# Kernel tuning notes

Hardware: AMD Instinct MI355X
Metric: run time of the kernel (lower is better)

Reference implementation:

```python
import jax, jax.numpy as jnp
import numpy as np

N_USER, N_ITEM, D, K, E = 80000, 40000, 128, 10, 2000000

def _mlp(x, w1, b1, w2, b2, w3, b3):
    # MLP from source: linear->tanh->linear->tanh->linear->L2 normalize (eval mode, dropout off)
    x = jnp.tanh(x @ w1 + b1)
    x = jnp.tanh(x @ w2 + b2)
    x = x @ w3 + b3
    return x / jnp.maximum(jnp.linalg.norm(x, axis=-1, keepdims=True), 1e-12)

def setup_inputs() -> dict:
    key = jax.random.key(0)
    ks = jax.random.split(key, 24)
    s = 0.05
    inp = {
        'uemb_s': jax.random.normal(ks[0], (N_USER, D), jnp.float32),
        'iemb_s': jax.random.normal(ks[1], (N_ITEM, D), jnp.float32),
        'uemb_t': jax.random.normal(ks[2], (N_USER, D), jnp.float32),
        'u_emb_sp': jax.random.normal(ks[3], (N_USER, D), jnp.float32),
        'edge_user': jax.random.randint(ks[4], (E,), 0, N_USER, jnp.int32),
        'edge_item': jax.random.randint(ks[5], (E,), 0, N_ITEM, jnp.int32),
        # meta nets
        'Wu': jax.random.normal(ks[6], (4 * D, D), jnp.float32) * s,
        'bu': jnp.zeros((D,), jnp.float32),
        'Wi': jax.random.normal(ks[7], (2 * D, D), jnp.float32) * s,
        'bi': jnp.zeros((D,), jnp.float32),
        # mlp1: D -> D*K -> D//2 -> D*K
        'm1w1': jax.random.normal(ks[8], (D, D * K), jnp.float32) * s,
        'm1b1': jnp.zeros((D * K,), jnp.float32),
        'm1w2': jax.random.normal(ks[9], (D * K, D // 2), jnp.float32) * s,
        'm1b2': jnp.zeros((D // 2,), jnp.float32),
        'm1w3': jax.random.normal(ks[10], (D // 2, D * K), jnp.float32) * s,
        'm1b3': jnp.zeros((D * K,), jnp.float32),
        # mlp2: D -> D*K -> D//2 -> D*K
        'm2w1': jax.random.normal(ks[11], (D, D * K), jnp.float32) * s,
        'm2b1': jnp.zeros((D * K,), jnp.float32),
        'm2w2': jax.random.normal(ks[12], (D * K, D // 2), jnp.float32) * s,
        'm2b2': jnp.zeros((D // 2,), jnp.float32),
        'm2w3': jax.random.normal(ks[13], (D // 2, D * K), jnp.float32) * s,
        'm2b3': jnp.zeros((D * K,), jnp.float32),
    }
    return inp

def reference(uemb_s, iemb_s, uemb_t, u_emb_sp, edge_user, edge_item,
              Wu, bu, Wi, bi,
              m1w1, m1b1, m1w2, m1b2, m1w3, m1b3,
              m2w1, m2b1, m2w2, m2b2, m2w3, m2b3):
    # spmm with all-ones values == gather + segment_sum over the bipartite edge list
    neighbors_u = jax.ops.segment_sum(iemb_s[edge_item], edge_user, num_segments=N_USER)  # [U, D]
    tmp_embu = jax.lax.stop_gradient(
        jnp.concatenate([uemb_s, uemb_t, u_emb_sp, neighbors_u], axis=1)) @ Wu + bu       # [U, D]
    neighbors_i = jax.ops.segment_sum(((uemb_s + u_emb_sp) * 0.5)[edge_user], edge_item,
                                      num_segments=N_ITEM)                               # [I, D]
    tmp_embi = jax.lax.stop_gradient(
        jnp.concatenate([iemb_s, neighbors_i], axis=1)) @ Wi + bi                         # [I, D]
    metau = _mlp(tmp_embu, m1w1, m1b1, m1w2, m1b2, m1w3, m1b3).reshape(-1, D, K)          # [U, D, K]
    metai = _mlp(tmp_embi, m2w1, m2b1, m2w2, m2b2, m2w3, m2b3).reshape(-1, K, D)          # [I, K, D]
    meta_biasu = jnp.mean(metau, axis=0)  # [D, K]
    meta_biasi = jnp.mean(metai, axis=0)  # [K, D]
    low_weightu = jax.nn.softmax(metau + meta_biasu, axis=1)
    low_weighti = jax.nn.softmax(metai + meta_biasi, axis=1)
    return (low_weightu, low_weighti)
```

## Files before the change

kernel.cpp:

```cpp
#include <hip/hip_runtime.h>
#include <hip/hip_bf16.h>

#define D_ 128
#define DK_ 1280
#define K_ 10

typedef __attribute__((ext_vector_type(8))) short bh8;
typedef __attribute__((ext_vector_type(4))) short bh4;
typedef __attribute__((ext_vector_type(4))) float f32x4;

__device__ __forceinline__ short f2b(float f) {
    unsigned u = __builtin_bit_cast(unsigned, f);
    u += 0x7fffu + ((u >> 16) & 1u);
    return (short)(u >> 16);
}
__device__ __forceinline__ float b2f(short s) {
    unsigned u = ((unsigned)(unsigned short)s) << 16;
    return __builtin_bit_cast(float, u);
}
__device__ __forceinline__ float tanh_fast(float x) {
    float e = __expf(2.f * x);
    return 1.f - __fdividef(2.f, e + 1.f);
}
__device__ __forceinline__ f32x4 mfma16(bh8 a, bh8 b, f32x4 c) {
    return __builtin_amdgcn_mfma_f32_16x16x32_bf16(a, b, c, 0, 0, 0);
}

__device__ __forceinline__ int blk_excl_scan(int v, int t) {
    __shared__ int wp[4];
    int lane = t & 63, w = t >> 6;
    int s = v;
    for (int o = 1; o < 64; o <<= 1) {
        int pv = __shfl_up(s, o);
        if (lane >= o) s += pv;
    }
    if (lane == 63) wp[w] = s;
    __syncthreads();
    if (t == 0) {
        int a = 0;
#pragma unroll
        for (int k = 0; k < 4; ++k) { int x = wp[k]; wp[k] = a; a += x; }
    }
    __syncthreads();
    int r = s - v + wp[w];
    __syncthreads();
    return r;
}

__global__ __launch_bounds__(256) void cvt_all(
    const float* __restrict__ us, const float* __restrict__ ut,
    const float* __restrict__ usp, const float* __restrict__ is_,
    short* __restrict__ usb, short* __restrict__ utb,
    short* __restrict__ uspb, short* __restrict__ uavg, short* __restrict__ isb,
    int n4u, int n4i)
{
    int i = blockIdx.x * 256 + threadIdx.x;
    if (i < n4u) {
        float4 a = ((const float4*)us)[i];
        float4 b = ((const float4*)ut)[i];
        float4 c = ((const float4*)usp)[i];
        bh4 sa, sb, sc, sv;
        sa[0] = f2b(a.x); sa[1] = f2b(a.y); sa[2] = f2b(a.z); sa[3] = f2b(a.w);
        sb[0] = f2b(b.x); sb[1] = f2b(b.y); sb[2] = f2b(b.z); sb[3] = f2b(b.w);
        sc[0] = f2b(c.x); sc[1] = f2b(c.y); sc[2] = f2b(c.z); sc[3] = f2b(c.w);
        sv[0] = f2b(0.5f * (a.x + c.x)); sv[1] = f2b(0.5f * (a.y + c.y));
        sv[2] = f2b(0.5f * (a.z + c.z)); sv[3] = f2b(0.5f * (a.w + c.w));
        ((bh4*)usb)[i] = sa; ((bh4*)utb)[i] = sb;
        ((bh4*)uspb)[i] = sc; ((bh4*)uavg)[i] = sv;
    } else if (i < n4u + n4i) {
        int j = i - n4u;
        float4 v = ((const float4*)is_)[j];
        bh4 s;
        s[0] = f2b(v.x); s[1] = f2b(v.y); s[2] = f2b(v.z); s[3] = f2b(v.w);
        ((bh4*)isb)[j] = s;
    }
}

struct PackArgs {
    const float* W[8];
    short* o[8];
    int K[8];
    int N[8];
};
__global__ __launch_bounds__(256) void pack_all(PackArgs pa)
{
    int seg = blockIdx.y;
    int K = pa.K[seg], N = pa.N[seg];
    int total = K * N;
    int o = blockIdx.x * 256 + threadIdx.x;
    if (o >= total) return;
    const float* W = pa.W[seg];
    short* out = pa.o[seg];
    int j    = o & 7;
    int lane = (o >> 3) & 63;
    int rest = o >> 9;
    int KK = K >> 5;
    int kk = rest % KK;
    int tile = rest / KK;
    int k = kk * 32 + (lane >> 4) * 8 + j;
    int n = tile * 16 + (lane & 15);
    out[o] = f2b(W[(size_t)k * N + n]);
}

__global__ __launch_bounds__(256) void bhist_kernel(
    const int* __restrict__ eu, const int* __restrict__ ei,
    int* __restrict__ bcu, int* __restrict__ bci,
    int E, int shu, int shi, int nbu, int nbi)
{
    __shared__ int hu[160], hi[160];
    int t = threadIdx.x;
    int base = blockIdx.x * 4096;
    if (t < 160) { hu[t] = 0; hi[t] = 0; }
    __syncthreads();
    int n = min(4096, E - base);
#pragma unroll 4
    for (int k = 0; k < 16; ++k) {
        int idx = k * 256 + t;
        if (idx < n) {
            atomicAdd(&hu[eu[base + idx] >> shu], 1);
            atomicAdd(&hi[ei[base + idx] >> shi], 1);
        }
    }
    __syncthreads();
    if (t < nbu && hu[t]) atomicAdd(&bcu[t], hu[t]);
    if (t < nbi && hi[t]) atomicAdd(&bci[t], hi[t]);
}

__global__ __launch_bounds__(256) void binit_kernel(
    const int* __restrict__ bcu, int* __restrict__ gcu, int* __restrict__ bbu, int nbu,
    const int* __restrict__ bci, int* __restrict__ gci, int* __restrict__ bbi, int nbi,
    int E)
{
    int t = threadIdx.x;
    {
        int v = (t < nbu) ? bcu[t] : 0;
        int ex = blk_excl_scan(v, t);
        if (t < nbu) { gcu[t] = ex; bbu[t] = ex; }
        if (t == 0) bbu[nbu] = E;
    }
    __syncthreads();
    {
        int v = (t < nbi) ? bci[t] : 0;
        int ex = blk_excl_scan(v, t);
        if (t < nbi) { gci[t] = ex; bbi[t] = ex; }
        if (t == 0) bbi[nbi] = E;
    }
}

__global__ __launch_bounds__(256) void partition_kernel(
    const int* __restrict__ eu, const int* __restrict__ ei,
    int* __restrict__ gcu, int* __restrict__ gci,
    uint2* __restrict__ ebu, uint2* __restrict__ ebi,
    int E, int shu, int shi, int nbu, int nbi)
{
    __shared__ int hu[160], hi[160];
    int t = threadIdx.x;
    int base = blockIdx.x * 4096;
    if (t < 160) { hu[t] = 0; hi[t] = 0; }
    __syncthreads();
    int n = min(4096, E - base);
    int us[16], is_[16];
#pragma unroll 4
    for (int k = 0; k < 16; ++k) {
        int idx = k * 256 + t;
        if (idx < n) {
            us[k] = eu[base + idx];
            is_[k] = ei[base + idx];
            atomicAdd(&hu[us[k] >> shu], 1);
            atomicAdd(&hi[is_[k] >> shi], 1);
        } else us[k] = -1;
    }
    __syncthreads();
    if (t < nbu) { int c = hu[t]; hu[t] = c ? atomicAdd(&gcu[t], c) : 0; }
    if (t < nbi) { int c = hi[t]; hi[t] = c ? atomicAdd(&gci[t], c) : 0; }
    __syncthreads();
#pragma unroll 4
    for (int k = 0; k < 16; ++k) {
        if (us[k] >= 0) {
            int p1 = atomicAdd(&hu[us[k] >> shu], 1);
            ebu[p1] = make_uint2((unsigned)us[k], (unsigned)is_[k]);
            int p2 = atomicAdd(&hi[is_[k] >> shi], 1);
            ebi[p2] = make_uint2((unsigned)is_[k], (unsigned)us[k]);
        }
    }
}

__global__ __launch_bounds__(256) void fill2_all(
    const uint2* __restrict__ ebu, const int* __restrict__ bbu,
    int* __restrict__ off_u, int* __restrict__ end_u, int* __restrict__ adj_u,
    int NBU, int U,
    const uint2* __restrict__ ebi, const int* __restrict__ bbi,
    int* __restrict__ off_i, int* __restrict__ end_i, int* __restrict__ adj_i, int I)
{
    __shared__ int lcnt[512];
    __shared__ int lcur[512];
    bool isU = (int)blockIdx.x < NBU;
    const uint2* ebuf = isU ? ebu : ebi;
    const int* bbase  = isU ? bbu : bbi;
    int* off  = isU ? off_u : off_i;
    int* end_ = isU ? end_u : end_i;
    int* adj  = isU ? adj_u : adj_i;
    int span_sh = isU ? 9 : 8;
    int nrows = isU ? U : I;
    int b = isU ? blockIdx.x : blockIdx.x - NBU;

    int t = threadIdx.x;
    int rbase = b << span_sh;
    int span = min(1 << span_sh, nrows - rbase);
    int regbeg = bbase[b], regend = bbase[b + 1];
    for (int j = t; j < span; j += 256) lcnt[j] = 0;
    __syncthreads();
    for (int e = regbeg + t; e < regend; e += 256)
        atomicAdd(&lcnt[ebuf[e].x - rbase], 1);
    __syncthreads();
    int c0 = (2 * t < span) ? lcnt[2 * t] : 0;
    int c1 = (2 * t + 1 < span) ? lcnt[2 * t + 1] : 0;
    int ex = blk_excl_scan(c0 + c1, t);
    if (2 * t < span) {
        int beg = regbeg + ex;
        off[rbase + 2 * t] = beg;
        end_[rbase + 2 * t] = beg + c0;
        lcur[2 * t] = beg;
    }
    if (2 * t + 1 < span) {
        int beg = regbeg + ex + c0;
        off[rbase + 2 * t + 1] = beg;
        end_[rbase + 2 * t + 1] = beg + c1;
        lcur[2 * t + 1] = beg;
    }
    __syncthreads();
    for (int e = regbeg + t; e < regend; e += 256) {
        uint2 p = ebuf[e];
        int slot = atomicAdd(&lcur[p.x - rbase], 1);
        adj[slot] = (int)p.y;
    }
}

__global__ __launch_bounds__(256) void gather_all(
    const short* __restrict__ embU, const short* __restrict__ embI,
    const int* __restrict__ off_u, const int* __restrict__ end_u, const int* __restrict__ adj_u,
    const int* __restrict__ off_i, const int* __restrict__ end_i, const int* __restrict__ adj_i,
    short* __restrict__ nub, short* __restrict__ nib, int U, int I)
{
    int gw = (blockIdx.x * 256 + threadIdx.x) >> 6;
    int lane = threadIdx.x & 63;
    const short* emb; const int *offp, *endp, *adjp; short* outp; int row;
    if (gw < U)          { emb = embU; offp = off_u; endp = end_u; adjp = adj_u; outp = nub; row = gw; }
    else if (gw < U + I) { emb = embI; offp = off_i; endp = end_i; adjp = adj_i; outp = nib; row = gw - U; }
    else return;

    int beg = offp[row], end = endp[row];
    float ax = 0.f, ay = 0.f;
    int j = beg;
    for (; j + 3 < end; j += 4) {
        unsigned a = *(const unsigned*)(emb + (size_t)adjp[j]     * D_ + lane * 2);
        unsigned b = *(const unsigned*)(emb + (size_t)adjp[j + 1] * D_ + lane * 2);
        unsigned c = *(const unsigned*)(emb + (size_t)adjp[j + 2] * D_ + lane * 2);
        unsigned d = *(const unsigned*)(emb + (size_t)adjp[j + 3] * D_ + lane * 2);
        ax += b2f((short)(a & 0xffff)) + b2f((short)(b & 0xffff))
            + b2f((short)(c & 0xffff)) + b2f((short)(d & 0xffff));
        ay += b2f((short)(a >> 16)) + b2f((short)(b >> 16))
            + b2f((short)(c >> 16)) + b2f((short)(d >> 16));
    }
    for (; j < end; ++j) {
        unsigned a = *(const unsigned*)(emb + (size_t)adjp[j] * D_ + lane * 2);
        ax += b2f((short)(a & 0xffff));
        ay += b2f((short)(a >> 16));
    }
    unsigned o = ((unsigned)(unsigned short)f2b(ay) << 16) | (unsigned short)(unsigned)f2b(ax);
    *(unsigned*)(outp + (size_t)row * D_ + lane * 2) = o;
}

struct MlpArgs {
    const short *uA0, *uA1, *uA2, *uA3;
    const short *iA0, *iA1;
    const short *uWg, *uW1, *uW2, *uW3;
    const short *iWg, *iW1, *iW2, *iW3;
    const float *ubg, *ub1, *ub2, *ub3;
    const float *ibg, *ib1, *ib2, *ib3;
    short *uY, *iY;
    float *uPart, *iPart;
    int UB;
};

__global__ __launch_bounds__(256, 3) void fused_mlp_all(MlpArgs P)
{
    __shared__ char pool[47104];
    __shared__ float wred[4][16];
    __shared__ float nrms[16];

    short* x2 = (short*)pool;
    short* xc = (short*)(pool + 4096);
    short* h1 = (short*)(pool + 4096);
    short* h2 = (short*)(pool + 45056);
    short* yb = (short*)pool;

    const int t = threadIdx.x;
    const int l = t & 63;
    const int w = t >> 6;
    const int lr = l & 15;
    const int lg = l >> 4;

    const bool isU = (int)blockIdx.x < P.UB;
    const int bid = isU ? (int)blockIdx.x : (int)blockIdx.x - P.UB;
    const size_t rb0 = (size_t)bid * 16;
    const int CHSH = isU ? 6 : 5;
    const int KKG  = isU ? 16 : 8;
    const short* Wg = isU ? P.uWg : P.iWg;
    const short* W1 = isU ? P.uW1 : P.iW1;
    const short* W2 = isU ? P.uW2 : P.iW2;
    const short* W3 = isU ? P.uW3 : P.iW3;
    const float* bg = isU ? P.ubg : P.ibg;
    const float* b1 = isU ? P.ub1 : P.ib1;
    const float* b2 = isU ? P.ub2 : P.ib2;
    const float* b3 = isU ? P.ub3 : P.ib3;
    short* Ybf = isU ? P.uY : P.iY;
    float* part = (isU ? P.uPart : P.iPart) + (size_t)bid * DK_;

    const int CH_ROW = 1 << CHSH;
    for (int idx = t; idx < (16 << CHSH); idx += 256) {
        int row = idx >> CHSH;
        int slot = idx & (CH_ROW - 1);
        int a = slot >> 4, cs = slot & 15;
        const short* src = isU ? (a == 0 ? P.uA0 : a == 1 ? P.uA1 : a == 2 ? P.uA2 : P.uA3)
                               : (a == 0 ? P.iA0 : P.iA1);
        bh8 v = *(const bh8*)(src + (rb0 + row) * D_ + cs * 8);
        int sl2 = slot ^ (row & 7);
        *(bh8*)(xc + (row << (CHSH + 3)) + sl2 * 8) = v;
    }
    __syncthreads();

    {
        f32x4 accA0 = {0,0,0,0}, accB0 = accA0, accA1 = accA0, accB1 = accA0;
#pragma unroll 4
        for (int kk = 0; kk < KKG; ++kk) {
            int slot = kk * 4 + lg;
            bh8 af = *(const bh8*)(xc + (lr << (CHSH + 3)) + ((slot ^ (lr & 7)) * 8));
            bh8 b0 = *(const bh8*)(Wg + (((size_t)(2 * w) * KKG + kk) * 64 + l) * 8);
            bh8 b1v = *(const bh8*)(Wg + (((size_t)(2 * w + 1) * KKG + kk) * 64 + l) * 8);
            if (kk & 1) { accB0 = mfma16(af, b0, accB0); accB1 = mfma16(af, b1v, accB1); }
            else        { accA0 = mfma16(af, b0, accA0); accA1 = mfma16(af, b1v, accA1); }
        }
#pragma unroll
        for (int r = 0; r < 4; ++r) {
            int row = lg * 4 + r;
            int c0 = (2 * w) * 16 + lr;
            int c1 = c0 + 16;
            x2[row * 128 + (((c0 >> 3) ^ (row & 7)) * 8) + (l & 7)] = f2b(accA0[r] + accB0[r] + bg[c0]);
            x2[row * 128 + (((c1 >> 3) ^ (row & 7)) * 8) + (l & 7)] = f2b(accA1[r] + accB1[r] + bg[c1]);
        }
    }
    __syncthreads();

    {
        bh8 a1f[4];
#pragma unroll
        for (int kk = 0; kk < 4; ++kk) {
            int slot = kk * 4 + lg;
            a1f[kk] = *(const bh8*)(x2 + lr * 128 + (slot ^ (lr & 7)) * 8);
        }
#pragma unroll 2
        for (int tile = w * 20; tile < w * 20 + 20; ++tile) {
            float bv = b1[tile * 16 + lr];
            f32x4 acc = {bv, bv, bv, bv};
#pragma unroll
            for (int kk = 0; kk < 4; ++kk) {
                bh8 bf_ = *(const bh8*)(W1 + (((size_t)tile * 4 + kk) * 64 + l) * 8);
                acc = mfma16(a1f[kk], bf_, acc);
            }
#pragma unroll
            for (int r = 0; r < 4; ++r) {
                int row = lg * 4 + r;
                int col = tile * 16 + lr;
                h1[row * 1280 + (((col >> 3) ^ (row & 7)) * 8) + (l & 7)] = f2b(tanh_fast(acc[r]));
            }
        }
    }
    __syncthreads();

    {
        float bv = b2[w * 16 + lr];
        f32x4 accA = {bv, bv, bv, bv}, accB = {0,0,0,0};
#pragma unroll 4
        for (int kk = 0; kk < 40; ++kk) {
            int slot = kk * 4 + lg;
            bh8 af = *(const bh8*)(h1 + lr * 1280 + (slot ^ (lr & 7)) * 8);
            bh8 bf_ = *(const bh8*)(W2 + (((size_t)w * 40 + kk) * 64 + l) * 8);
            if (kk & 1) accB = mfma16(af, bf_, accB);
            else        accA = mfma16(af, bf_, accA);
        }
#pragma unroll
        for (int r = 0; r < 4; ++r) {
            int row = lg * 4 + r;
            int col = w * 16 + lr;
            h2[row * 64 + (((col >> 3) ^ (row & 7)) * 8) + (l & 7)] = f2b(tanh_fast(accA[r] + accB[r]));
        }
    }
    __syncthreads();

    {
        bh8 a3[2];
#pragma unroll
        for (int kk = 0; kk < 2; ++kk) {
            int slot = kk * 4 + lg;
            a3[kk] = *(const bh8*)(h2 + lr * 64 + (slot ^ (lr & 7)) * 8);
        }
        float ssq[4] = {0.f, 0.f, 0.f, 0.f};
#pragma unroll 2
        for (int tile = w * 20; tile < w * 20 + 20; ++tile) {
            float bv = b3[tile * 16 + lr];
            f32x4 acc = {bv, bv, bv, bv};
            bh8 b0 = *(const bh8*)(W3 + (((size_t)tile * 2 + 0) * 64 + l) * 8);
            bh8 b1v = *(const bh8*)(W3 + (((size_t)tile * 2 + 1) * 64 + l) * 8);
            acc = mfma16(a3[0], b0, acc);
            acc = mfma16(a3[1], b1v, acc);
            bh4 pk;
#pragma unroll
            for (int r = 0; r < 4; ++r) {
                ssq[r] = fmaf(acc[r], acc[r], ssq[r]);
                pk[r] = f2b(acc[r]);
            }
            *(bh4*)(yb + tile * 260 + l * 4) = pk;
        }
#pragma unroll
        for (int off = 1; off < 16; off <<= 1) {
#pragma unroll
            for (int r = 0; r < 4; ++r) ssq[r] += __shfl_xor(ssq[r], off);
        }
        if (lr == 0) {
#pragma unroll
            for (int r = 0; r < 4; ++r) wred[w][lg * 4 + r] = ssq[r];
        }
    }
    __syncthreads();
    if (t < 16) {
        float s = wred[0][t] + wred[1][t] + wred[2][t] + wred[3][t];
        nrms[t] = 1.f / fmaxf(sqrtf(s), 1e-12f);
    }
    __syncthreads();

    {
        float csum[5] = {0.f, 0.f, 0.f, 0.f, 0.f};
        for (int row = 0; row < 16; ++row) {
            float nv = nrms[row];
            int lph = (row >> 2) << 4;
            int r = row & 3;
#pragma unroll
            for (int ch = 0; ch < 5; ++ch) {
                int c = ch * 256 + t;
                int tile = c >> 4;
                int lanep = lph | (c & 15);
                float v = b2f(yb[tile * 260 + lanep * 4 + r]) * nv;
                Ybf[(rb0 + row) * DK_ + c] = f2b(v);
                csum[ch] += v;
            }
        }
#pragma unroll
        for (int ch = 0; ch < 5; ++ch) part[ch * 256 + t] = csum[ch];
    }
}

__global__ __launch_bounds__(256) void finalize_bias(
    const float* __restrict__ partU, const float* __restrict__ partI,
    float* __restrict__ bsu, float* __restrict__ bsi, int NU, int NI)
{
    int c = blockIdx.x * 256 + threadIdx.x;
    int z = blockIdx.z;
    const float* part = z ? partI : partU;
    float* dst = z ? bsi : bsu;
    int M = z ? NI : NU;
    int chunk = (M + gridDim.y - 1) / gridDim.y;
    int r0 = blockIdx.y * chunk;
    int r1 = min(M, r0 + chunk);
    if (r0 >= r1) return;
    float s = 0.f;
    for (int r = r0; r < r1; ++r) s += part[(size_t)r * DK_ + c];
    atomicAdd(&dst[c], s);
}

__global__ __launch_bounds__(64) void softmax_all(
    const short* __restrict__ Yu, const short* __restrict__ Yi,
    const float* __restrict__ bsu, const float* __restrict__ bsi,
    float invU, float invI,
    float* __restrict__ outu, float* __restrict__ outi, int U, int I)
{
    __shared__ float rowb[DK_];
    int b = blockIdx.x;
    int t = threadIdx.x;
    if (b < U) {
        size_t base = (size_t)b * DK_;
        for (int i = t; i < DK_ / 4; i += 64) {
            uint2 a = ((const uint2*)(Yu + base))[i];
            float4 bv = ((const float4*)bsu)[i];
            rowb[4 * i + 0] = b2f((short)(a.x & 0xffff)) + bv.x * invU;
            rowb[4 * i + 1] = b2f((short)(a.x >> 16))    + bv.y * invU;
            rowb[4 * i + 2] = b2f((short)(a.y & 0xffff)) + bv.z * invU;
            rowb[4 * i + 3] = b2f((short)(a.y >> 16))    + bv.w * invU;
        }
        __syncthreads();
#pragma unroll 1
        for (int k = 0; k < K_; ++k) {
            float v0 = rowb[t * K_ + k];
            float v1 = rowb[(t + 64) * K_ + k];
            float m = fmaxf(v0, v1);
            for (int off = 32; off; off >>= 1) m = fmaxf(m, __shfl_xor(m, off));
            float e0 = expf(v0 - m), e1 = expf(v1 - m);
            float s = e0 + e1;
            for (int off = 32; off; off >>= 1) s += __shfl_xor(s, off);
            float rs = 1.f / s;
            rowb[t * K_ + k] = e0 * rs;
            rowb[(t + 64) * K_ + k] = e1 * rs;
        }
        __syncthreads();
        for (int i = t; i < DK_ / 4; i += 64)
            ((float4*)(outu + base))[i] = ((const float4*)rowb)[i];
    } else {
        int it = b - U;
        if (it >= I) return;
        size_t base = (size_t)it * DK_;
        float v0[K_], v1[K_];
        float m0 = -1e30f, m1 = -1e30f;
#pragma unroll
        for (int k = 0; k < K_; ++k) {
            unsigned a = *(const unsigned*)(Yi + base + k * D_ + 2 * t);
            float2 bv = ((const float2*)(bsi + k * D_))[t];
            v0[k] = b2f((short)(a & 0xffff)) + bv.x * invI;
            v1[k] = b2f((short)(a >> 16))    + bv.y * invI;
            m0 = fmaxf(m0, v0[k]); m1 = fmaxf(m1, v1[k]);
        }
        float s0 = 0.f, s1 = 0.f;
#pragma unroll
        for (int k = 0; k < K_; ++k) {
            v0[k] = expf(v0[k] - m0); s0 += v0[k];
            v1[k] = expf(v1[k] - m1); s1 += v1[k];
        }
        float r0 = 1.f / s0, r1 = 1.f / s1;
#pragma unroll
        for (int k = 0; k < K_; ++k) {
            float2 o; o.x = v0[k] * r0; o.y = v1[k] * r1;
            ((float2*)(outi + base + k * D_))[t] = o;
        }
    }
}

extern "C" void kernel_launch(void* const* d_in, const int* in_sizes, int n_in,
                              void* d_out, int out_size, void* d_ws, size_t ws_size,
                              hipStream_t stream)
{
    const float* uemb_s   = (const float*)d_in[0];
    const float* iemb_s   = (const float*)d_in[1];
    const float* uemb_t   = (const float*)d_in[2];
    const float* u_emb_sp = (const float*)d_in[3];
    const int*   eu       = (const int*)d_in[4];
    const int*   ei       = (const int*)d_in[5];
    const float* Wu  = (const float*)d_in[6];
    const float* bu  = (const float*)d_in[7];
    const float* Wi  = (const float*)d_in[8];
    const float* bi  = (const float*)d_in[9];
    const float* m1w1 = (const float*)d_in[10];
    const float* m1b1 = (const float*)d_in[11];
    const float* m1w2 = (const float*)d_in[12];
    const float* m1b2 = (const float*)d_in[13];
    const float* m1w3 = (const float*)d_in[14];
    const float* m1b3 = (const float*)d_in[15];
    const float* m2w1 = (const float*)d_in[16];
    const float* m2b1 = (const float*)d_in[17];
    const float* m2w2 = (const float*)d_in[18];
    const float* m2b2 = (const float*)d_in[19];
    const float* m2w3 = (const float*)d_in[20];
    const float* m2b3 = (const float*)d_in[21];

    const int U = in_sizes[0] / D_;
    const int I = in_sizes[1] / D_;
    const int E = in_sizes[4];

    const int SHU = 9, SHI = 8;
    const int NBU = (U + 511) >> 9;
    const int NBI = (I + 255) >> 8;
    const int UB = U / 16, IB = I / 16;

    char* p = (char*)d_ws;
    auto alloc = [&](size_t bytes) { char* r = p; p += (bytes + 255) & ~(size_t)255; return r; };

    short* usb  = (short*)alloc((size_t)U * D_ * 2);
    short* utb  = (short*)alloc((size_t)U * D_ * 2);
    short* uspb = (short*)alloc((size_t)U * D_ * 2);
    short* uavg = (short*)alloc((size_t)U * D_ * 2);
    short* isb  = (short*)alloc((size_t)I * D_ * 2);
    short* nub  = (short*)alloc((size_t)U * D_ * 2);
    short* nib  = (short*)alloc((size_t)I * D_ * 2);
    short* ybu  = (short*)alloc((size_t)U * DK_ * 2);
    short* ybi  = (short*)alloc((size_t)I * DK_ * 2);
    float* partU = (float*)alloc((size_t)UB * DK_ * 4);
    float* partI = (float*)alloc((size_t)IB * DK_ * 4);
    short* WgU  = (short*)alloc(512 * 128 * 2);
    short* WgI  = (short*)alloc(256 * 128 * 2);
    short* W1U  = (short*)alloc(128 * 1280 * 2);
    short* W2U  = (short*)alloc(1280 * 64 * 2);
    short* W3U  = (short*)alloc(64 * 1280 * 2);
    short* W1I  = (short*)alloc(128 * 1280 * 2);
    short* W2I  = (short*)alloc(1280 * 64 * 2);
    short* W3I  = (short*)alloc(64 * 1280 * 2);
    int*   zbuf = (int*)alloc((320 + 2 * DK_) * 4);
    int* bcnt_u = zbuf;
    int* bcnt_i = zbuf + 160;
    float* bsu  = (float*)(zbuf + 320);
    float* bsi  = bsu + DK_;
    int* gcur_u = (int*)alloc(160 * 4);
    int* gcur_i = (int*)alloc(160 * 4);
    int* bbase_u = (int*)alloc(161 * 4);
    int* bbase_i = (int*)alloc(161 * 4);
    int* off_u  = (int*)alloc((size_t)U * 4);
    int* end_u  = (int*)alloc((size_t)U * 4);
    int* off_i  = (int*)alloc((size_t)I * 4);
    int* end_i  = (int*)alloc((size_t)I * 4);
    uint2* ebu  = (uint2*)alloc((size_t)E * 8);
    uint2* ebi  = (uint2*)alloc((size_t)E * 8);
    int* adj_u  = (int*)alloc((size_t)E * 4);
    int* adj_i  = (int*)alloc((size_t)E * 4);

    float* outu = (float*)d_out;
    float* outi = outu + (size_t)U * DK_;

    hipMemsetAsync(zbuf, 0, (320 + 2 * DK_) * 4, stream);

    int n4u = U * D_ / 4, n4i = I * D_ / 4;
    cvt_all<<<(n4u + n4i + 255) / 256, 256, 0, stream>>>(
        uemb_s, uemb_t, u_emb_sp, iemb_s, usb, utb, uspb, uavg, isb, n4u, n4i);

    PackArgs pa;
    pa.W[0] = Wu;   pa.o[0] = WgU; pa.K[0] = 512;  pa.N[0] = 128;
    pa.W[1] = Wi;   pa.o[1] = WgI; pa.K[1] = 256;  pa.N[1] = 128;
    pa.W[2] = m1w1; pa.o[2] = W1U; pa.K[2] = 128;  pa.N[2] = 1280;
    pa.W[3] = m1w2; pa.o[3] = W2U; pa.K[3] = 1280; pa.N[3] = 64;
    pa.W[4] = m1w3; pa.o[4] = W3U; pa.K[4] = 64;   pa.N[4] = 1280;
    pa.W[5] = m2w1; pa.o[5] = W1I; pa.K[5] = 128;  pa.N[5] = 1280;
    pa.W[6] = m2w2; pa.o[6] = W2I; pa.K[6] = 1280; pa.N[6] = 64;
    pa.W[7] = m2w3; pa.o[7] = W3I; pa.K[7] = 64;   pa.N[7] = 1280;
    pack_all<<<dim3(640, 8), 256, 0, stream>>>(pa);

    int pb = (E + 4095) / 4096;
    bhist_kernel<<<pb, 256, 0, stream>>>(eu, ei, bcnt_u, bcnt_i, E, SHU, SHI, NBU, NBI);
    binit_kernel<<<1, 256, 0, stream>>>(bcnt_u, gcur_u, bbase_u, NBU,
                                        bcnt_i, gcur_i, bbase_i, NBI, E);
    partition_kernel<<<pb, 256, 0, stream>>>(eu, ei, gcur_u, gcur_i, ebu, ebi,
                                             E, SHU, SHI, NBU, NBI);
    fill2_all<<<NBU + NBI, 256, 0, stream>>>(ebu, bbase_u, off_u, end_u, adj_u, NBU, U,
                                             ebi, bbase_i, off_i, end_i, adj_i, I);

    gather_all<<<(U + I + 3) / 4, 256, 0, stream>>>(
        isb, uavg, off_u, end_u, adj_u, off_i, end_i, adj_i, nub, nib, U, I);

    MlpArgs ma;
    ma.uA0 = usb; ma.uA1 = utb; ma.uA2 = uspb; ma.uA3 = nub;
    ma.iA0 = isb; ma.iA1 = nib;
    ma.uWg = WgU; ma.uW1 = W1U; ma.uW2 = W2U; ma.uW3 = W3U;
    ma.iWg = WgI; ma.iW1 = W1I; ma.iW2 = W2I; ma.iW3 = W3I;
    ma.ubg = bu; ma.ub1 = m1b1; ma.ub2 = m1b2; ma.ub3 = m1b3;
    ma.ibg = bi; ma.ib1 = m2b1; ma.ib2 = m2b2; ma.ib3 = m2b3;
    ma.uY = ybu; ma.iY = ybi;
    ma.uPart = partU; ma.iPart = partI;
    ma.UB = UB;
    fused_mlp_all<<<UB + IB, 256, 0, stream>>>(ma);

    finalize_bias<<<dim3(5, 40, 2), 256, 0, stream>>>(partU, partI, bsu, bsi, UB, IB);

    softmax_all<<<U + I, 64, 0, stream>>>(ybu, ybi, bsu, bsi,
                                          1.0f / (float)U, 1.0f / (float)I, outu, outi, U, I);
}
```

Measured before the change: 880.4 us.

## Transpose MFMA operands, use padded LDS layouts, and compute bias sums from Y

The fused MLP kernel now swaps MFMA operand order so each lane holds 4 consecutive output columns of one row. It replaces the XOR-swizzled LDS layouts with padded strides, which allows packed bh4 stores and a simpler norm reduction. The per-block partial column sums are gone, and finalize_bias instead re-reads the bf16 Y output over 256 row chunks and adds the results atomically. This removes the partial buffer traffic and the strided epilogue, but the bias pass now reads the full Y array again and sums bf16-rounded values instead of fp32 ones.

```diff
diff --git a/kernel.cpp b/kernel.cpp
--- a/kernel.cpp
+++ b/kernel.cpp
@@ -279,21 +279,21 @@
     const float *ubg, *ub1, *ub2, *ub3;
     const float *ibg, *ib1, *ib2, *ib3;
     short *uY, *iY;
-    float *uPart, *iPart;
     int UB;
 };
 
+#define X2ST 136
+#define H1ST 1288
+#define H2ST 72
+
 __global__ __launch_bounds__(256, 3) void fused_mlp_all(MlpArgs P)
 {
-    __shared__ char pool[47104];
-    __shared__ float wred[4][16];
-    __shared__ float nrms[16];
-
-    short* x2 = (short*)pool;
-    short* xc = (short*)(pool + 4096);
-    short* h1 = (short*)(pool + 4096);
-    short* h2 = (short*)(pool + 45056);
-    short* yb = (short*)pool;
+    __shared__ char pool[48128];
+    short* x2   = (short*)pool;
+    short* h2   = (short*)(pool + 4352);
+    float* wred = (float*)(pool + 6656);
+    short* xc   = (short*)(pool + 6912);
+    short* h1   = (short*)(pool + 6912);
 
     const int t = threadIdx.x;
     const int l = t & 63;
@@ -306,6 +306,7 @@
     const size_t rb0 = (size_t)bid * 16;
     const int CHSH = isU ? 6 : 5;
     const int KKG  = isU ? 16 : 8;
+    const int XST  = isU ? 520 : 264;
     const short* Wg = isU ? P.uWg : P.iWg;
     const short* W1 = isU ? P.uW1 : P.iW1;
     const short* W2 = isU ? P.uW2 : P.iW2;
@@ -315,18 +316,15 @@
     const float* b2 = isU ? P.ub2 : P.ib2;
     const float* b3 = isU ? P.ub3 : P.ib3;
     short* Ybf = isU ? P.uY : P.iY;
-    float* part = (isU ? P.uPart : P.iPart) + (size_t)bid * DK_;
-
-    const int CH_ROW = 1 << CHSH;
+
     for (int idx = t; idx < (16 << CHSH); idx += 256) {
         int row = idx >> CHSH;
-        int slot = idx & (CH_ROW - 1);
+        int slot = idx & ((1 << CHSH) - 1);
         int a = slot >> 4, cs = slot & 15;
         const short* src = isU ? (a == 0 ? P.uA0 : a == 1 ? P.uA1 : a == 2 ? P.uA2 : P.uA3)
                                : (a == 0 ? P.iA0 : P.iA1);
         bh8 v = *(const bh8*)(src + (rb0 + row) * D_ + cs * 8);
-        int sl2 = slot ^ (row & 7);
-        *(bh8*)(xc + (row << (CHSH + 3)) + sl2 * 8) = v;
+        *(bh8*)(xc + row * XST + slot * 8) = v;
     }
     __syncthreads();
 
@@ -334,148 +332,133 @@
         f32x4 accA0 = {0,0,0,0}, accB0 = accA0, accA1 = accA0, accB1 = accA0;
 #pragma unroll 4
         for (int kk = 0; kk < KKG; ++kk) {
-            int slot = kk * 4 + lg;
-            bh8 af = *(const bh8*)(xc + (lr << (CHSH + 3)) + ((slot ^ (lr & 7)) * 8));
-            bh8 b0 = *(const bh8*)(Wg + (((size_t)(2 * w) * KKG + kk) * 64 + l) * 8);
-            bh8 b1v = *(const bh8*)(Wg + (((size_t)(2 * w + 1) * KKG + kk) * 64 + l) * 8);
-            if (kk & 1) { accB0 = mfma16(af, b0, accB0); accB1 = mfma16(af, b1v, accB1); }
-            else        { accA0 = mfma16(af, b0, accA0); accA1 = mfma16(af, b1v, accA1); }
-        }
+            bh8 xf = *(const bh8*)(xc + lr * XST + kk * 32 + lg * 8);
+            bh8 w0 = *(const bh8*)(Wg + (((size_t)(2 * w)     * KKG + kk) * 64 + l) * 8);
+            bh8 w1 = *(const bh8*)(Wg + (((size_t)(2 * w + 1) * KKG + kk) * 64 + l) * 8);
+            if (kk & 1) { accB0 = mfma16(w0, xf, accB0); accB1 = mfma16(w1, xf, accB1); }
+            else        { accA0 = mfma16(w0, xf, accA0); accA1 = mfma16(w1, xf, accA1); }
+        }
+        const float* bp0 = bg + (2 * w) * 16 + lg * 4;
+        const float* bp1 = bg + (2 * w + 1) * 16 + lg * 4;
+        bh4 p0, p1;
 #pragma unroll
         for (int r = 0; r < 4; ++r) {
-            int row = lg * 4 + r;
-            int c0 = (2 * w) * 16 + lr;
-            int c1 = c0 + 16;
-            x2[row * 128 + (((c0 >> 3) ^ (row & 7)) * 8) + (l & 7)] = f2b(accA0[r] + accB0[r] + bg[c0]);
-            x2[row * 128 + (((c1 >> 3) ^ (row & 7)) * 8) + (l & 7)] = f2b(accA1[r] + accB1[r] + bg[c1]);
-        }
+            p0[r] = f2b(accA0[r] + accB0[r] + bp0[r]);
+            p1[r] = f2b(accA1[r] + accB1[r] + bp1[r]);
+        }
+        *(bh4*)(x2 + lr * X2ST + (2 * w) * 16 + lg * 4) = p0;
+        *(bh4*)(x2 + lr * X2ST + (2 * w + 1) * 16 + lg * 4) = p1;
     }
     __syncthreads();
 
     {
-        bh8 a1f[4];
-#pragma unroll
-        for (int kk = 0; kk < 4; ++kk) {
-            int slot = kk * 4 + lg;
-            a1f[kk] = *(const bh8*)(x2 + lr * 128 + (slot ^ (lr & 7)) * 8);
-        }
+        bh8 xf[4];
+#pragma unroll
+        for (int kk = 0; kk < 4; ++kk)
+            xf[kk] = *(const bh8*)(x2 + lr * X2ST + kk * 32 + lg * 8);
 #pragma unroll 2
         for (int tile = w * 20; tile < w * 20 + 20; ++tile) {
-            float bv = b1[tile * 16 + lr];
-            f32x4 acc = {bv, bv, bv, bv};
+            f32x4 acc = {0, 0, 0, 0};
 #pragma unroll
             for (int kk = 0; kk < 4; ++kk) {
-                bh8 bf_ = *(const bh8*)(W1 + (((size_t)tile * 4 + kk) * 64 + l) * 8);
-                acc = mfma16(a1f[kk], bf_, acc);
+                bh8 wf = *(const bh8*)(W1 + (((size_t)tile * 4 + kk) * 64 + l) * 8);
+                acc = mfma16(wf, xf[kk], acc);
             }
-#pragma unroll
-            for (int r = 0; r < 4; ++r) {
-                int row = lg * 4 + r;
-                int col = tile * 16 + lr;
-                h1[row * 1280 + (((col >> 3) ^ (row & 7)) * 8) + (l & 7)] = f2b(tanh_fast(acc[r]));
-            }
+            const float* bp = b1 + tile * 16 + lg * 4;
+            bh4 pk;
+#pragma unroll
+            for (int r = 0; r < 4; ++r) pk[r] = f2b(tanh_fast(acc[r] + bp[r]));
+            *(bh4*)(h1 + lr * H1ST + tile * 16 + lg * 4) = pk;
         }
     }
     __syncthreads();
 
     {
-        float bv = b2[w * 16 + lr];
-        f32x4 accA = {bv, bv, bv, bv}, accB = {0,0,0,0};
+        f32x4 accA = {0,0,0,0}, accB = accA;
 #pragma unroll 4
         for (int kk = 0; kk < 40; ++kk) {
-            int slot = kk * 4 + lg;
-            bh8 af = *(const bh8*)(h1 + lr * 1280 + (slot ^ (lr & 7)) * 8);
-            bh8 bf_ = *(const bh8*)(W2 + (((size_t)w * 40 + kk) * 64 + l) * 8);
-            if (kk & 1) accB = mfma16(af, bf_, accB);
-            else        accA = mfma16(af, bf_, accA);
-        }
-#pragma unroll
-        for (int r = 0; r < 4; ++r) {
-            int row = lg * 4 + r;
-            int col = w * 16 + lr;
-            h2[row * 64 + (((col >> 3) ^ (row & 7)) * 8) + (l & 7)] = f2b(tanh_fast(accA[r] + accB[r]));
-        }
+            bh8 hf = *(const bh8*)(h1 + lr * H1ST + kk * 32 + lg * 8);
+            bh8 wf = *(const bh8*)(W2 + (((size_t)w * 40 + kk) * 64 + l) * 8);
+            if (kk & 1) accB = mfma16(wf, hf, accB);
+            else        accA = mfma16(wf, hf, accA);
+        }
+        const float* bp = b2 + w * 16 + lg * 4;
+        bh4 pk;
+#pragma unroll
+        for (int r = 0; r < 4; ++r) pk[r] = f2b(tanh_fast(accA[r] + accB[r] + bp[r]));
+        *(bh4*)(h2 + lr * H2ST + w * 16 + lg * 4) = pk;
     }
     __syncthreads();
 
     {
-        bh8 a3[2];
-#pragma unroll
-        for (int kk = 0; kk < 2; ++kk) {
-            int slot = kk * 4 + lg;
-            a3[kk] = *(const bh8*)(h2 + lr * 64 + (slot ^ (lr & 7)) * 8);
-        }
-        float ssq[4] = {0.f, 0.f, 0.f, 0.f};
+        bh8 hf0 = *(const bh8*)(h2 + lr * H2ST + lg * 8);
+        bh8 hf1 = *(const bh8*)(h2 + lr * H2ST + 32 + lg * 8);
+        float ssq = 0.f;
 #pragma unroll 2
         for (int tile = w * 20; tile < w * 20 + 20; ++tile) {
-            float bv = b3[tile * 16 + lr];
-            f32x4 acc = {bv, bv, bv, bv};
-            bh8 b0 = *(const bh8*)(W3 + (((size_t)tile * 2 + 0) * 64 + l) * 8);
-            bh8 b1v = *(const bh8*)(W3 + (((size_t)tile * 2 + 1) * 64 + l) * 8);
-            acc = mfma16(a3[0], b0, acc);
-            acc = mfma16(a3[1], b1v, acc);
+            f32x4 acc = {0, 0, 0, 0};
+            bh8 w0 = *(const bh8*)(W3 + (((size_t)tile * 2 + 0) * 64 + l) * 8);
+            bh8 w1 = *(const bh8*)(W3 + (((size_t)tile * 2 + 1) * 64 + l) * 8);
+            acc = mfma16(w0, hf0, acc);
+            acc = mfma16(w1, hf1, acc);
+            const float* bp = b3 + tile * 16 + lg * 4;
             bh4 pk;
 #pragma unroll
             for (int r = 0; r < 4; ++r) {
-                ssq[r] = fmaf(acc[r], acc[r], ssq[r]);
-                pk[r] = f2b(acc[r]);
+                float v = acc[r] + bp[r];
+                ssq = fmaf(v, v, ssq);
+                pk[r] = f2b(v);
             }
-            *(bh4*)(yb + tile * 260 + l * 4) = pk;
-        }
-#pragma unroll
-        for (int off = 1; off < 16; off <<= 1) {
-#pragma unroll
-            for (int r = 0; r < 4; ++r) ssq[r] += __shfl_xor(ssq[r], off);
-        }
-        if (lr == 0) {
-#pragma unroll
-            for (int r = 0; r < 4; ++r) wred[w][lg * 4 + r] = ssq[r];
-        }
-    }
-    __syncthreads();
-    if (t < 16) {
-        float s = wred[0][t] + wred[1][t] + wred[2][t] + wred[3][t];
-        nrms[t] = 1.f / fmaxf(sqrtf(s), 1e-12f);
+            *(bh4*)(h1 + lr * H1ST + tile * 16 + lg * 4) = pk;
+        }
+        ssq += __shfl_xor(ssq, 16);
+        ssq += __shfl_xor(ssq, 32);
+        if (l < 16) wred[w * 16 + l] = ssq;
     }
     __syncthreads();
 
     {
-        float csum[5] = {0.f, 0.f, 0.f, 0.f, 0.f};
-        for (int row = 0; row < 16; ++row) {
-            float nv = nrms[row];
-            int lph = (row >> 2) << 4;
-            int r = row & 3;
-#pragma unroll
-            for (int ch = 0; ch < 5; ++ch) {
-                int c = ch * 256 + t;
-                int tile = c >> 4;
-                int lanep = lph | (c & 15);
-                float v = b2f(yb[tile * 260 + lanep * 4 + r]) * nv;
-                Ybf[(rb0 + row) * DK_ + c] = f2b(v);
-                csum[ch] += v;
-            }
-        }
-#pragma unroll
-        for (int ch = 0; ch < 5; ++ch) part[ch * 256 + t] = csum[ch];
+        float s = wred[lr] + wred[16 + lr] + wred[32 + lr] + wred[48 + lr];
+        float nrm = 1.f / fmaxf(sqrtf(s), 1e-12f);
+        short* dst = Ybf + (rb0 + lr) * DK_;
+#pragma unroll 2
+        for (int tile = w * 20; tile < w * 20 + 20; ++tile) {
+            bh4 pk = *(const bh4*)(h1 + lr * H1ST + tile * 16 + lg * 4);
+            bh4 o;
+#pragma unroll
+            for (int r = 0; r < 4; ++r) o[r] = f2b(b2f(pk[r]) * nrm);
+            *(bh4*)(dst + tile * 16 + lg * 4) = o;
+        }
     }
 }
 
 __global__ __launch_bounds__(256) void finalize_bias(
-    const float* __restrict__ partU, const float* __restrict__ partI,
-    float* __restrict__ bsu, float* __restrict__ bsi, int NU, int NI)
-{
-    int c = blockIdx.x * 256 + threadIdx.x;
-    int z = blockIdx.z;
-    const float* part = z ? partI : partU;
+    const short* __restrict__ Yu, const short* __restrict__ Yi,
+    float* __restrict__ bsu, float* __restrict__ bsi, int U, int I, int NCH)
+{
+    int z = blockIdx.y;
+    const short* Y = z ? Yi : Yu;
     float* dst = z ? bsi : bsu;
-    int M = z ? NI : NU;
-    int chunk = (M + gridDim.y - 1) / gridDim.y;
-    int r0 = blockIdx.y * chunk;
+    int M = z ? I : U;
+    int chunk = (M + NCH - 1) / NCH;
+    int r0 = blockIdx.x * chunk;
     int r1 = min(M, r0 + chunk);
     if (r0 >= r1) return;
-    float s = 0.f;
-    for (int r = r0; r < r1; ++r) s += part[(size_t)r * DK_ + c];
-    atomicAdd(&dst[c], s);
+    int t = threadIdx.x;
+    float s0 = 0.f, s1 = 0.f, s2 = 0.f, s3 = 0.f, s4 = 0.f;
+    for (int r = r0; r < r1; ++r) {
+        const short* row = Y + (size_t)r * DK_;
+        s0 += b2f(row[t]);
+        s1 += b2f(row[256 + t]);
+        s2 += b2f(row[512 + t]);
+        s3 += b2f(row[768 + t]);
+        s4 += b2f(row[1024 + t]);
+    }
+    atomicAdd(&dst[t], s0);
+    atomicAdd(&dst[256 + t], s1);
+    atomicAdd(&dst[512 + t], s2);
+    atomicAdd(&dst[768 + t], s3);
+    atomicAdd(&dst[1024 + t], s4);
 }
 
 __global__ __launch_bounds__(64) void softmax_all(
@@ -591,8 +574,6 @@
     short* nib  = (short*)alloc((size_t)I * D_ * 2);
     short* ybu  = (short*)alloc((size_t)U * DK_ * 2);
     short* ybi  = (short*)alloc((size_t)I * DK_ * 2);
-    float* partU = (float*)alloc((size_t)UB * DK_ * 4);
-    float* partI = (float*)alloc((size_t)IB * DK_ * 4);
     short* WgU  = (short*)alloc(512 * 128 * 2);
     short* WgI  = (short*)alloc(256 * 128 * 2);
     short* W1U  = (short*)alloc(128 * 1280 * 2);
@@ -659,11 +640,10 @@
     ma.ubg = bu; ma.ub1 = m1b1; ma.ub2 = m1b2; ma.ub3 = m1b3;
     ma.ibg = bi; ma.ib1 = m2b1; ma.ib2 = m2b2; ma.ib3 = m2b3;
     ma.uY = ybu; ma.iY = ybi;
-    ma.uPart = partU; ma.iPart = partI;
     ma.UB = UB;
     fused_mlp_all<<<UB + IB, 256, 0, stream>>>(ma);
 
-    finalize_bias<<<dim3(5, 40, 2), 256, 0, stream>>>(partU, partI, bsu, bsi, UB, IB);
+    finalize_bias<<<dim3(256, 2), 256, 0, stream>>>(ybu, ybi, bsu, bsi, U, I, 256);
 
     softmax_all<<<U + I, 64, 0, stream>>>(ybu, ybi, bsu, bsi,
                                           1.0f / (float)U, 1.0f / (float)I, outu, outi, U, I);
```

Result: slower. 1.027 ms (+16.7%).
